# Kernel tuning notes

Hardware: AMD Instinct MI355X
Metric: run time of the kernel (lower is better)

## Reference

```python
import jax, jax.numpy as jnp
import numpy as np

N_NODES = 40000
N_EDGES = 640000
F_IN = 128
F_OUT = 128
K_HOPS = 2


def setup_inputs() -> dict:
    key = jax.random.key(0)
    k1, k2, k3, k4 = jax.random.split(key, 4)
    x = jax.random.normal(k1, (N_NODES, F_IN), dtype=jnp.float32)
    edge_index = jax.random.randint(k2, (2, N_EDGES), 0, N_NODES, dtype=jnp.int64)
    edge_weight = jax.random.uniform(k3, (N_EDGES,), dtype=jnp.float32)
    # Linear(in_feats, out_feats): weight [F_OUT, F_IN], bias [F_OUT]
    W = jax.random.normal(k4, (F_OUT, F_IN), dtype=jnp.float32) * (1.0 / np.sqrt(F_IN))
    b = jnp.zeros((F_OUT,), dtype=jnp.float32)
    return {"x": x, "edge_index": edge_index, "edge_weight": edge_weight, "W": W, "b": b}


def reference(x, edge_index, edge_weight, W, b):
    N = x.shape[0]
    # gcn_norm with add_self_loops=True, fill_value=1.0
    loop = jnp.arange(N, dtype=edge_index.dtype)
    row = jnp.concatenate([edge_index[0], loop])  # source (j)
    col = jnp.concatenate([edge_index[1], loop])  # target (i)
    w = jnp.concatenate([edge_weight, jnp.ones((N,), dtype=edge_weight.dtype)])
    deg = jax.ops.segment_sum(w, col, num_segments=N)
    deg_inv_sqrt = jnp.where(deg > 0, jax.lax.rsqrt(jnp.maximum(deg, 1e-30)), 0.0)
    norm = deg_inv_sqrt[row] * w * deg_inv_sqrt[col]  # [E+N]
    # K-hop propagation: x <- A_norm @ x, repeated K times
    for _ in range(K_HOPS):
        msgs = norm[:, None] * x[row]  # [E+N, F]
        x = jax.ops.segment_sum(msgs, col, num_segments=N)
    # final linear
    return x @ W.T + b
```

## Files before the change

### kernel.cpp

```cpp
#include <hip/hip_runtime.h>
#include <hip/hip_fp16.h>


#define F   128
#define CAP 64

typedef _Float16 f16x8 __attribute__((ext_vector_type(8)));
typedef float    f32x4 __attribute__((ext_vector_type(4)));

__global__ __launch_bounds__(256) void prep_kernel(
    const float2* __restrict__ x2in, __half2* __restrict__ xh, int npairs,
    const int* __restrict__ ei, const float* __restrict__ ew,
    int* __restrict__ cnt, unsigned int* __restrict__ bucket, int E,
    const float2* __restrict__ W2, __half2* __restrict__ Wh2,
    int buildBlocks, int cvtBlocks) {
    int b = blockIdx.x;
    if (b < buildBlocks) {
        int idx = b * 256 + threadIdx.x;
        int half = E >> 1;
        if (idx >= half) return;
        int e0 = idx, e1 = idx + half;
        int r0 = ei[e0], c0 = ei[E + e0]; float w0 = ew[e0];
        int r1 = ei[e1], c1 = ei[E + e1]; float w1 = ew[e1];
        int p0 = atomicAdd(&cnt[(size_t)c0 << 3], 1);
        int p1 = atomicAdd(&cnt[(size_t)c1 << 3], 1);
        if (p0 < CAP) {
            unsigned short hw = __half_as_ushort(__float2half(w0));
            bucket[c0 * CAP + p0] = (unsigned int)r0 | ((unsigned int)hw << 16);
        }
        if (p1 < CAP) {
            unsigned short hw = __half_as_ushort(__float2half(w1));
            bucket[c1 * CAP + p1] = (unsigned int)r1 | ((unsigned int)hw << 16);
        }
    } else if (b < buildBlocks + cvtBlocks) {
        int idx = (b - buildBlocks) * 256 + threadIdx.x;
        if (idx < npairs) xh[idx] = __float22half2_rn(x2in[idx]);
    } else {
        int idx = (b - buildBlocks - cvtBlocks) * 256 + threadIdx.x;
        if (idx < F * F / 2) Wh2[idx] = __float22half2_rn(W2[idx]);
    }
}

__global__ __launch_bounds__(256) void deg_dinv_kernel(
    const unsigned int* __restrict__ bucket, const int* __restrict__ cnt,
    float* __restrict__ dinv, int N) {
    int lane = threadIdx.x & 63;
    int wid  = threadIdx.x >> 6;
    int i = blockIdx.x * 4 + wid;
    if (i >= N) return;
    int c = min(cnt[(size_t)i << 3], CAP);
    float w = 0.0f;
    if (lane < c) {
        unsigned int ent = bucket[i * CAP + lane];
        w = __half2float(__ushort_as_half((unsigned short)(ent >> 16)));
    }
    #pragma unroll
    for (int off = 32; off >= 1; off >>= 1) w += __shfl_xor(w, off, 64);
    if (lane == 0) dinv[i] = 1.0f / sqrtf(w + 1.0f);
}

__global__ __launch_bounds__(256) void hop_kernel(
    const unsigned short* __restrict__ xin, unsigned short* __restrict__ xout,
    const float* __restrict__ dinv, const unsigned int* __restrict__ bucket,
    const int* __restrict__ cnt) {
    int t = threadIdx.x;
    int lane = t & 63;
    int wid  = t >> 6;
    int q = lane & 31;
    int h = lane >> 5;
    int i = blockIdx.x * 8 + wid * 2 + h;

    int c = min(cnt[(size_t)i << 3], CAP);
    float di = dinv[i];
    int r0 = i, r1 = i;
    float n0 = 0.0f, n1 = 0.0f;
    if (q < c) {
        unsigned int ent = bucket[i * CAP + q];
        r0 = (int)(ent & 0xFFFFu);
        float w = __half2float(__ushort_as_half((unsigned short)(ent >> 16)));
        n0 = di * dinv[r0] * w;
    }
    if (q + 32 < c) {
        unsigned int ent = bucket[i * CAP + q + 32];
        r1 = (int)(ent & 0xFFFFu);
        float w = __half2float(__ushort_as_half((unsigned short)(ent >> 16)));
        n1 = di * dinv[r1] * w;
    }
    int cmax = max(c, __shfl_xor(c, 32, 64));

    uint2 sv = *(const uint2*)(xin + (size_t)i * F + q * 4);
    float2 slo = __half22float2(*(const __half2*)&sv.x);
    float2 shi = __half22float2(*(const __half2*)&sv.y);
    float dii = di * di;
    float4 acc = make_float4(dii * slo.x, dii * slo.y, dii * shi.x, dii * shi.y);

    int kend1 = cmax < 32 ? cmax : 32;
    int k = 0;
    for (; k + 8 <= kend1; k += 8) {
        int rr[8]; float nn[8]; uint2 v[8];
        #pragma unroll
        for (int j = 0; j < 8; ++j) {
            rr[j] = __shfl(r0, k + j, 32);
            nn[j] = __shfl(n0, k + j, 32);
        }
        #pragma unroll
        for (int j = 0; j < 8; ++j)
            v[j] = *(const uint2*)(xin + (size_t)rr[j] * F + q * 4);
        #pragma unroll
        for (int j = 0; j < 8; ++j) {
            float2 lo = __half22float2(*(const __half2*)&v[j].x);
            float2 hi = __half22float2(*(const __half2*)&v[j].y);
            acc.x += nn[j] * lo.x; acc.y += nn[j] * lo.y;
            acc.z += nn[j] * hi.x; acc.w += nn[j] * hi.y;
        }
    }
    for (; k < kend1; ++k) {
        int   rk = __shfl(r0, k, 32);
        float nk = __shfl(n0, k, 32);
        uint2 v  = *(const uint2*)(xin + (size_t)rk * F + q * 4);
        float2 lo = __half22float2(*(const __half2*)&v.x);
        float2 hi = __half22float2(*(const __half2*)&v.y);
        acc.x += nk * lo.x; acc.y += nk * lo.y;
        acc.z += nk * hi.x; acc.w += nk * hi.y;
    }
    for (; k + 8 <= cmax; k += 8) {
        int rr[8]; float nn[8]; uint2 v[8];
        #pragma unroll
        for (int j = 0; j < 8; ++j) {
            rr[j] = __shfl(r1, k - 32 + j, 32);
            nn[j] = __shfl(n1, k - 32 + j, 32);
        }
        #pragma unroll
        for (int j = 0; j < 8; ++j)
            v[j] = *(const uint2*)(xin + (size_t)rr[j] * F + q * 4);
        #pragma unroll
        for (int j = 0; j < 8; ++j) {
            float2 lo = __half22float2(*(const __half2*)&v[j].x);
            float2 hi = __half22float2(*(const __half2*)&v[j].y);
            acc.x += nn[j] * lo.x; acc.y += nn[j] * lo.y;
            acc.z += nn[j] * hi.x; acc.w += nn[j] * hi.y;
        }
    }
    for (; k < cmax; ++k) {
        int   rk = __shfl(r1, k - 32, 32);
        float nk = __shfl(n1, k - 32, 32);
        uint2 v  = *(const uint2*)(xin + (size_t)rk * F + q * 4);
        float2 lo = __half22float2(*(const __half2*)&v.x);
        float2 hi = __half22float2(*(const __half2*)&v.y);
        acc.x += nk * lo.x; acc.y += nk * lo.y;
        acc.z += nk * hi.x; acc.w += nk * hi.y;
    }

    uint2 o;
    *(__half2*)&o.x = __float22half2_rn(make_float2(acc.x, acc.y));
    *(__half2*)&o.y = __float22half2_rn(make_float2(acc.z, acc.w));
    *(uint2*)&xout[(size_t)i * F + q * 4] = o;
}

__global__ __launch_bounds__(256) void linear_mfma_kernel(
    const unsigned short* __restrict__ x2h, const unsigned short* __restrict__ Wh,
    const float* __restrict__ bias, float* __restrict__ out) {
    int t = threadIdx.x;
    int lane = t & 63;
    int wid  = t >> 6;
    int m    = lane & 15;
    int quad = lane >> 4;
    int n0 = blockIdx.x * 64 + wid * 16;

    f32x4 acc[8];
    #pragma unroll
    for (int ft = 0; ft < 8; ++ft) acc[ft] = (f32x4){0.f, 0.f, 0.f, 0.f};

    #pragma unroll
    for (int ks = 0; ks < 4; ++ks) {
        f16x8 a = *(const f16x8*)(x2h + (size_t)(n0 + m) * F + ks * 32 + quad * 8);
        #pragma unroll
        for (int ft = 0; ft < 8; ++ft) {
            f16x8 b = *(const f16x8*)(Wh + (size_t)(ft * 16 + m) * F + ks * 32 + quad * 8);
            acc[ft] = __builtin_amdgcn_mfma_f32_16x16x32_f16(a, b, acc[ft], 0, 0, 0);
        }
    }
    #pragma unroll
    for (int ft = 0; ft < 8; ++ft) {
        int f = ft * 16 + m;
        float bv = bias[f];
        #pragma unroll
        for (int reg = 0; reg < 4; ++reg) {
            int n = n0 + quad * 4 + reg;
            out[(size_t)n * F + f] = acc[ft][reg] + bv;
        }
    }
}

extern "C" void kernel_launch(void* const* d_in, const int* in_sizes, int n_in,
                              void* d_out, int out_size, void* d_ws, size_t ws_size,
                              hipStream_t stream) {
    const float* x    = (const float*)d_in[0];
    const int*   ei   = (const int*)d_in[1];
    const float* ew   = (const float*)d_in[2];
    const float* W    = (const float*)d_in[3];
    const float* bias = (const float*)d_in[4];
    float* out = (float*)d_out;

    const int N = in_sizes[0] / F;
    const int E = in_sizes[2];

    char* ws = (char*)d_ws;
    size_t off = 0;
    auto take = [&](size_t bytes) {
        size_t r = off;
        off = (off + bytes + 255) & ~(size_t)255;
        return r;
    };
    size_t o_cnt    = take((size_t)N * 32);
    size_t zero_end = off;
    size_t o_dinv   = take((size_t)N * 4);
    size_t o_bucket = take((size_t)N * CAP * 4);
    size_t o_xh     = take((size_t)N * F * 2);
    size_t o_x1h    = take((size_t)N * F * 2);
    size_t o_x2h    = take((size_t)N * F * 2);
    size_t o_wh     = take((size_t)F * F * 2);
    (void)o_cnt; (void)ws_size;

    int*            cnt    = (int*)(ws);
    float*          dinv   = (float*)(ws + o_dinv);
    unsigned int*   bucket = (unsigned int*)(ws + o_bucket);
    __half2*        xh2    = (__half2*)(ws + o_xh);
    unsigned short* xh     = (unsigned short*)(ws + o_xh);
    unsigned short* x1h    = (unsigned short*)(ws + o_x1h);
    unsigned short* x2h    = (unsigned short*)(ws + o_x2h);
    __half2*        wh2    = (__half2*)(ws + o_wh);
    unsigned short* wh     = (unsigned short*)(ws + o_wh);

    hipMemsetAsync(ws, 0, zero_end, stream);

    int npairs = N * 64;
    int buildBlocks = (E / 2 + 255) / 256;
    int cvtBlocks   = (npairs + 255) / 256;
    int wBlocks     = (F * F / 2 + 255) / 256;
    prep_kernel<<<buildBlocks + cvtBlocks + wBlocks, 256, 0, stream>>>(
        (const float2*)x, xh2, npairs, ei, ew, cnt, bucket, E,
        (const float2*)W, wh2, buildBlocks, cvtBlocks);
    deg_dinv_kernel<<<N / 4, 256, 0, stream>>>(bucket, cnt, dinv, N);
    hop_kernel<<<N / 8, 256, 0, stream>>>(xh,  x1h, dinv, bucket, cnt);
    hop_kernel<<<N / 8, 256, 0, stream>>>(x1h, x2h, dinv, bucket, cnt);
    linear_mfma_kernel<<<N / 64, 256, 0, stream>>>(x2h, wh, bias, out);
}
```

Measured before the change: 186.0 us.

## Build CSR buckets via two-pass shared-memory binning instead of global atomics

The edge-bucket build now runs in two passes. First, each block groups its 4096 edges into coarse bins of 256 target nodes using shared-memory atomics. A finalize kernel then scatters each bin into per-node buckets and sums the degrees in shared memory. This removes the global atomics on padded counters, the memset and the separate degree kernel. The cost is an extra intermediate buffer and a finalize stage with only about 157 blocks, which limits parallelism. Edges beyond the per-bin cap of 64 would be silently dropped.

```diff
diff --git a/kernel.cpp b/kernel.cpp
--- a/kernel.cpp
+++ b/kernel.cpp
@@ -2,8 +2,10 @@
 #include <hip/hip_fp16.h>
 
 
-#define F   128
-#define CAP 64
+#define F    128
+#define CAP  64
+#define EPB  4096
+#define BPT  16
 
 typedef _Float16 f16x8 __attribute__((ext_vector_type(8)));
 typedef float    f32x4 __attribute__((ext_vector_type(4)));
@@ -11,27 +13,43 @@
 __global__ __launch_bounds__(256) void prep_kernel(
     const float2* __restrict__ x2in, __half2* __restrict__ xh, int npairs,
     const int* __restrict__ ei, const float* __restrict__ ew,
-    int* __restrict__ cnt, unsigned int* __restrict__ bucket, int E,
+    uint2* __restrict__ coarse, int* __restrict__ cnt1, int E,
+    int nbin, int nb1,
     const float2* __restrict__ W2, __half2* __restrict__ Wh2,
     int buildBlocks, int cvtBlocks) {
     int b = blockIdx.x;
     if (b < buildBlocks) {
-        int idx = b * 256 + threadIdx.x;
-        int half = E >> 1;
-        if (idx >= half) return;
-        int e0 = idx, e1 = idx + half;
-        int r0 = ei[e0], c0 = ei[E + e0]; float w0 = ew[e0];
-        int r1 = ei[e1], c1 = ei[E + e1]; float w1 = ew[e1];
-        int p0 = atomicAdd(&cnt[(size_t)c0 << 3], 1);
-        int p1 = atomicAdd(&cnt[(size_t)c1 << 3], 1);
-        if (p0 < CAP) {
-            unsigned short hw = __half_as_ushort(__float2half(w0));
-            bucket[c0 * CAP + p0] = (unsigned int)r0 | ((unsigned int)hw << 16);
-        }
-        if (p1 < CAP) {
-            unsigned short hw = __half_as_ushort(__float2half(w1));
-            bucket[c1 * CAP + p1] = (unsigned int)r1 | ((unsigned int)hw << 16);
-        }
+        __shared__ int binCnt[256];
+        int t = threadIdx.x;
+        if (t < nbin) binCnt[t] = 0;
+        __syncthreads();
+        int base = b * EPB;
+        unsigned rc[BPT]; unsigned short hw[BPT];
+        #pragma unroll
+        for (int j = 0; j < BPT; ++j) {
+            int e = base + j * 256 + t;
+            bool v = e < E;
+            int   r = v ? ei[e]     : 0;
+            int   c = v ? ei[E + e] : 0;
+            float w = v ? ew[e]     : 0.f;
+            rc[j] = v ? ((unsigned)r | ((unsigned)c << 16)) : 0xFFFFFFFFu;
+            hw[j] = __half_as_ushort(__float2half(w));
+        }
+        #pragma unroll
+        for (int j = 0; j < BPT; ++j) {
+            if (rc[j] == 0xFFFFFFFFu) continue;
+            int c   = (int)(rc[j] >> 16);
+            int bin = c >> 8;
+            int rank = atomicAdd(&binCnt[bin], 1);
+            if (rank < CAP) {
+                uint2 ent;
+                ent.x = (rc[j] & 0xFFFFu) | ((unsigned)hw[j] << 16);
+                ent.y = (unsigned)(c & 0xFF);
+                coarse[((size_t)bin * nb1 + b) * CAP + rank] = ent;
+            }
+        }
+        __syncthreads();
+        if (t < nbin) cnt1[(size_t)b * nbin + t] = min(binCnt[t], CAP);
     } else if (b < buildBlocks + cvtBlocks) {
         int idx = (b - buildBlocks) * 256 + threadIdx.x;
         if (idx < npairs) xh[idx] = __float22half2_rn(x2in[idx]);
@@ -41,22 +59,38 @@
     }
 }
 
-__global__ __launch_bounds__(256) void deg_dinv_kernel(
-    const unsigned int* __restrict__ bucket, const int* __restrict__ cnt,
-    float* __restrict__ dinv, int N) {
-    int lane = threadIdx.x & 63;
-    int wid  = threadIdx.x >> 6;
-    int i = blockIdx.x * 4 + wid;
-    if (i >= N) return;
-    int c = min(cnt[(size_t)i << 3], CAP);
-    float w = 0.0f;
-    if (lane < c) {
-        unsigned int ent = bucket[i * CAP + lane];
-        w = __half2float(__ushort_as_half((unsigned short)(ent >> 16)));
-    }
-    #pragma unroll
-    for (int off = 32; off >= 1; off >>= 1) w += __shfl_xor(w, off, 64);
-    if (lane == 0) dinv[i] = 1.0f / sqrtf(w + 1.0f);
+__global__ __launch_bounds__(256) void finalize_kernel(
+    const uint2* __restrict__ coarse, const int* __restrict__ cnt1,
+    unsigned int* __restrict__ bucket, int* __restrict__ cnt,
+    float* __restrict__ dinv, int N, int nbin, int nb1) {
+    __shared__ int   nodeCnt[256];
+    __shared__ float degS[256];
+    __shared__ int   c1s[256];
+    int b = blockIdx.x;
+    int t = threadIdx.x;
+    nodeCnt[t] = 0;
+    degS[t]    = 0.f;
+    for (int i = t; i < nb1; i += 256) c1s[i] = cnt1[(size_t)i * nbin + b];
+    __syncthreads();
+    int tot = nb1 * CAP;
+    for (int s = t; s < tot; s += 256) {
+        int blk = s >> 6, slot = s & 63;
+        if (slot < c1s[blk]) {
+            uint2 ent = coarse[((size_t)b * nb1 + blk) * CAP + slot];
+            int local = (int)(ent.y & 0xFFu);
+            int rank  = atomicAdd(&nodeCnt[local], 1);
+            float wf  = __half2float(__ushort_as_half((unsigned short)(ent.x >> 16)));
+            atomicAdd(&degS[local], wf);
+            if (rank < CAP)
+                bucket[(((size_t)b << 8) | (unsigned)local) * CAP + rank] = ent.x;
+        }
+    }
+    __syncthreads();
+    int node = (b << 8) + t;
+    if (node < N) {
+        cnt[node]  = min(nodeCnt[t], CAP);
+        dinv[node] = 1.0f / sqrtf(degS[t] + 1.0f);
+    }
 }
 
 __global__ __launch_bounds__(256) void hop_kernel(
@@ -70,7 +104,7 @@
     int h = lane >> 5;
     int i = blockIdx.x * 8 + wid * 2 + h;
 
-    int c = min(cnt[(size_t)i << 3], CAP);
+    int c = min(cnt[i], CAP);
     float di = dinv[i];
     int r0 = i, r1 = i;
     float n0 = 0.0f, n1 = 0.0f;
@@ -205,6 +239,9 @@
     const int N = in_sizes[0] / F;
     const int E = in_sizes[2];
 
+    const int nbin = (N + 255) >> 8;
+    const int nb1  = (E + EPB - 1) / EPB;
+
     char* ws = (char*)d_ws;
     size_t off = 0;
     auto take = [&](size_t bytes) {
@@ -212,17 +249,20 @@
         off = (off + bytes + 255) & ~(size_t)255;
         return r;
     };
-    size_t o_cnt    = take((size_t)N * 32);
-    size_t zero_end = off;
+    size_t o_cnt1   = take((size_t)nb1 * nbin * 4);
+    size_t o_coarse = take((size_t)nbin * nb1 * CAP * 8);
+    size_t o_cnt    = take((size_t)N * 4);
     size_t o_dinv   = take((size_t)N * 4);
     size_t o_bucket = take((size_t)N * CAP * 4);
     size_t o_xh     = take((size_t)N * F * 2);
     size_t o_x1h    = take((size_t)N * F * 2);
     size_t o_x2h    = take((size_t)N * F * 2);
     size_t o_wh     = take((size_t)F * F * 2);
-    (void)o_cnt; (void)ws_size;
-
-    int*            cnt    = (int*)(ws);
+    (void)ws_size;
+
+    int*            cnt1   = (int*)(ws + o_cnt1);
+    uint2*          coarse = (uint2*)(ws + o_coarse);
+    int*            cnt    = (int*)(ws + o_cnt);
     float*          dinv   = (float*)(ws + o_dinv);
     unsigned int*   bucket = (unsigned int*)(ws + o_bucket);
     __half2*        xh2    = (__half2*)(ws + o_xh);
@@ -232,16 +272,14 @@
     __half2*        wh2    = (__half2*)(ws + o_wh);
     unsigned short* wh     = (unsigned short*)(ws + o_wh);
 
-    hipMemsetAsync(ws, 0, zero_end, stream);
-
     int npairs = N * 64;
-    int buildBlocks = (E / 2 + 255) / 256;
-    int cvtBlocks   = (npairs + 255) / 256;
-    int wBlocks     = (F * F / 2 + 255) / 256;
-    prep_kernel<<<buildBlocks + cvtBlocks + wBlocks, 256, 0, stream>>>(
-        (const float2*)x, xh2, npairs, ei, ew, cnt, bucket, E,
-        (const float2*)W, wh2, buildBlocks, cvtBlocks);
-    deg_dinv_kernel<<<N / 4, 256, 0, stream>>>(bucket, cnt, dinv, N);
+    int cvtBlocks = (npairs + 255) / 256;
+    int wBlocks   = (F * F / 2 + 255) / 256;
+    prep_kernel<<<nb1 + cvtBlocks + wBlocks, 256, 0, stream>>>(
+        (const float2*)x, xh2, npairs, ei, ew, coarse, cnt1, E, nbin, nb1,
+        (const float2*)W, wh2, nb1, cvtBlocks);
+    finalize_kernel<<<nbin, 256, 0, stream>>>(coarse, cnt1, bucket, cnt, dinv,
+                                              N, nbin, nb1);
     hop_kernel<<<N / 8, 256, 0, stream>>>(xh,  x1h, dinv, bucket, cnt);
     hop_kernel<<<N / 8, 256, 0, stream>>>(x1h, x2h, dinv, bucket, cnt);
     linear_mfma_kernel<<<N / 64, 256, 0, stream>>>(x2h, wh, bias, out);
```

After: 173.6 us. -6.6%, faster.
